# Kernel optimization log

Hardware: AMD Instinct MI355X
Metric: run time of the kernel (lower is better)

The kernel has to match this reference:

```python
import jax, jax.numpy as jnp
import numpy as np

NODE_DIM = 256
HIDDEN = 64
NUM_REL = 10
N_NODES = 100000
N_EDGES = 1600000


def _linear_params(key, fan_in, fan_out):
    kw, kb = jax.random.split(key)
    bound = 1.0 / np.sqrt(fan_in)
    W = jax.random.uniform(kw, (fan_in, fan_out), minval=-bound, maxval=bound, dtype=jnp.float32)
    b = jax.random.uniform(kb, (fan_out,), minval=-bound, maxval=bound, dtype=jnp.float32)
    return W, b


def setup_inputs() -> dict:
    key = jax.random.key(0)
    ks = jax.random.split(key, 6)
    x = jax.random.normal(ks[0], (N_NODES, NODE_DIM), dtype=jnp.float32)
    edge_index = jax.random.randint(ks[1], (2, N_EDGES), 0, N_NODES, dtype=jnp.int32)
    W1, b1 = _linear_params(ks[2], NODE_DIM, HIDDEN)   # node_encoder layer 1
    W2, b2 = _linear_params(ks[3], HIDDEN, HIDDEN)     # node_encoder layer 2
    W3, b3 = _linear_params(ks[4], 2 * HIDDEN, HIDDEN) # relation_mlp layer 1
    W4, b4 = _linear_params(ks[5], HIDDEN, NUM_REL)    # relation_mlp layer 2
    return {"x": x, "edge_index": edge_index,
            "W1": W1, "b1": b1, "W2": W2, "b2": b2,
            "W3": W3, "b3": b3, "W4": W4, "b4": b4}


def reference(x, edge_index, W1, b1, W2, b2, W3, b3, W4, b4):
    # node encoder: Linear -> ReLU -> Linear, [N, node_dim] -> [N, H]
    h = jax.nn.relu(x @ W1 + b1) @ W2 + b2
    row, col = edge_index[0], edge_index[1]
    # gather + concat: [E, 2H]
    edge_features = jnp.concatenate([h[row], h[col]], axis=-1)
    # relation MLP: [E, 2H] -> [E, num_relations]
    relation_logits = jax.nn.relu(edge_features @ W3 + b3) @ W4 + b4
    relation_probs = jax.nn.softmax(relation_logits, axis=-1)
    edge_type = jnp.argmax(relation_logits, axis=-1)
    return edge_type, relation_probs
```

## Files before the change

### kernel.cpp

```cpp
#include <hip/hip_runtime.h>

#define NODE_DIM 256
#define HIDDEN 64
#define NUM_REL 10

#define FMA4(A, S, W) do { \
    (A).x = fmaf((S), (W).x, (A).x); \
    (A).y = fmaf((S), (W).y, (A).y); \
    (A).z = fmaf((S), (W).z, (A).z); \
    (A).w = fmaf((S), (W).w, (A).w); } while (0)

#define ELEM(V, I) ((I) == 0 ? (V).x : (I) == 1 ? (V).y : (I) == 2 ? (V).z : (V).w)

__global__ __launch_bounds__(256) void node_kernel(
    const float* __restrict__ x,
    const float* __restrict__ W1, const float* __restrict__ b1,
    const float* __restrict__ W2, const float* __restrict__ b2,
    const float* __restrict__ W3,
    float* __restrict__ Hout, float* __restrict__ Aout, int N)
{
    int n = blockIdx.x * 256 + threadIdx.x;
    if (n >= N) return;

    float h1[64];
    #pragma unroll
    for (int j = 0; j < 64; ++j) h1[j] = 0.0f;

    const float4* xr = (const float4*)(x + (size_t)n * NODE_DIM);
    #pragma unroll 1
    for (int k4 = 0; k4 < NODE_DIM / 4; ++k4) {
        float4 xv = xr[k4];
        const float* w = W1 + (size_t)k4 * 4 * 64;
        #pragma unroll
        for (int j = 0; j < 64; ++j) h1[j] = fmaf(xv.x, w[j], h1[j]);
        #pragma unroll
        for (int j = 0; j < 64; ++j) h1[j] = fmaf(xv.y, w[64 + j], h1[j]);
        #pragma unroll
        for (int j = 0; j < 64; ++j) h1[j] = fmaf(xv.z, w[128 + j], h1[j]);
        #pragma unroll
        for (int j = 0; j < 64; ++j) h1[j] = fmaf(xv.w, w[192 + j], h1[j]);
    }
    #pragma unroll
    for (int j = 0; j < 64; ++j) h1[j] = fmaxf(h1[j] + b1[j], 0.0f);

    float h[64];
    #pragma unroll
    for (int c = 0; c < 4; ++c) {
        float acc[16];
        #pragma unroll
        for (int j = 0; j < 16; ++j) acc[j] = 0.0f;
        #pragma unroll
        for (int k = 0; k < 64; ++k) {
            const float* w = W2 + (size_t)k * 64 + c * 16;
            #pragma unroll
            for (int j = 0; j < 16; ++j) acc[j] = fmaf(h1[k], w[j], acc[j]);
        }
        #pragma unroll
        for (int j = 0; j < 16; ++j) h[c * 16 + j] = acc[j] + b2[c * 16 + j];
    }

    float4* hr = (float4*)(Hout + (size_t)n * 64);
    #pragma unroll
    for (int j4 = 0; j4 < 16; ++j4) {
        float4 v;
        v.x = h[4 * j4]; v.y = h[4 * j4 + 1];
        v.z = h[4 * j4 + 2]; v.w = h[4 * j4 + 3];
        hr[j4] = v;
    }

    float4* ar = (float4*)(Aout + (size_t)n * 64);
    #pragma unroll
    for (int c = 0; c < 4; ++c) {
        float acc[16];
        #pragma unroll
        for (int j = 0; j < 16; ++j) acc[j] = 0.0f;
        #pragma unroll
        for (int k = 0; k < 64; ++k) {
            const float* w = W3 + (size_t)k * 64 + c * 16;
            #pragma unroll
            for (int j = 0; j < 16; ++j) acc[j] = fmaf(h[k], w[j], acc[j]);
        }
        #pragma unroll
        for (int j4 = 0; j4 < 4; ++j4) {
            float4 v;
            v.x = acc[4 * j4]; v.y = acc[4 * j4 + 1];
            v.z = acc[4 * j4 + 2]; v.w = acc[4 * j4 + 3];
            ar[c * 4 + j4] = v;
        }
    }
}

__global__ __launch_bounds__(256, 4) void edge_kernel(
    const int* __restrict__ ei,
    const float* __restrict__ H, const float* __restrict__ A,
    const float* __restrict__ W3, const float* __restrict__ b3,
    const float* __restrict__ W4, const float* __restrict__ b4,
    float* __restrict__ out_type, float* __restrict__ out_probs, int E)
{
    __shared__ float4 HcS[256 * 8];

    const int tid = threadIdx.x;
    const int e = blockIdx.x * 256 + tid;
    const bool valid = (e < E);
    const int sw = tid & 7;
    float4* myscr = &HcS[tid * 8];

    const int c = valid ? ei[E + e] : 0;
    const int r = valid ? ei[e] : 0;
    const float4* src = (const float4*)(H + (size_t)c * 64);
    const float4* Ar  = (const float4*)(A + (size_t)r * 64);

    #pragma unroll
    for (int q = 0; q < 8; ++q) myscr[q ^ sw] = src[q];

    float4 acc[16];
    #pragma unroll
    for (int j = 0; j < 16; ++j) acc[j] = Ar[j];

    const float* W3b = W3 + 64 * 64;

    #pragma unroll 1
    for (int k4 = 0; k4 < 8; ++k4) {
        const float4 hv = myscr[k4 ^ sw];
        #pragma unroll
        for (int i = 0; i < 4; ++i) {
            const float s = ELEM(hv, i);
            const float* w = W3b + (size_t)(k4 * 4 + i) * 64;
            #pragma unroll
            for (int j = 0; j < 16; ++j) {
                float4 wv = *(const float4*)(w + 4 * j);
                FMA4(acc[j], s, wv);
            }
        }
    }

    #pragma unroll
    for (int q = 0; q < 8; ++q) myscr[q ^ sw] = src[8 + q];

    #pragma unroll 1
    for (int k4 = 8; k4 < 16; ++k4) {
        const float4 hv = myscr[(k4 - 8) ^ sw];
        #pragma unroll
        for (int i = 0; i < 4; ++i) {
            const float s = ELEM(hv, i);
            const float* w = W3b + (size_t)(k4 * 4 + i) * 64;
            #pragma unroll
            for (int j = 0; j < 16; ++j) {
                float4 wv = *(const float4*)(w + 4 * j);
                FMA4(acc[j], s, wv);
            }
        }
    }

    #pragma unroll
    for (int j = 0; j < 16; ++j) {
        float4 bv = *(const float4*)(b3 + 4 * j);
        acc[j].x = fmaxf(acc[j].x + bv.x, 0.f);
        acc[j].y = fmaxf(acc[j].y + bv.y, 0.f);
        acc[j].z = fmaxf(acc[j].z + bv.z, 0.f);
        acc[j].w = fmaxf(acc[j].w + bv.w, 0.f);
    }

    float lg[NUM_REL];
    #pragma unroll
    for (int j = 0; j < NUM_REL; ++j) lg[j] = 0.0f;
    #pragma unroll
    for (int jq = 0; jq < 16; ++jq) {
        #pragma unroll
        for (int i = 0; i < 4; ++i) {
            const float s = ELEM(acc[jq], i);
            const float* w = W4 + (size_t)(jq * 4 + i) * NUM_REL;
            #pragma unroll
            for (int j = 0; j < NUM_REL; ++j) lg[j] = fmaf(s, w[j], lg[j]);
        }
    }

    if (!valid) return;

    #pragma unroll
    for (int j = 0; j < NUM_REL; ++j) lg[j] += b4[j];

    int best = 0;
    float bm = lg[0];
    #pragma unroll
    for (int j = 1; j < NUM_REL; ++j)
        if (lg[j] > bm) { bm = lg[j]; best = j; }

    float p[NUM_REL];
    float sum = 0.0f;
    #pragma unroll
    for (int j = 0; j < NUM_REL; ++j) {
        p[j] = expf(lg[j] - bm);
        sum += p[j];
    }
    float inv = 1.0f / sum;

    out_type[e] = (float)best;
    float* op = out_probs + (size_t)e * NUM_REL;
    #pragma unroll
    for (int j = 0; j < NUM_REL; ++j) op[j] = p[j] * inv;
}

extern "C" void kernel_launch(void* const* d_in, const int* in_sizes, int n_in,
                              void* d_out, int out_size, void* d_ws, size_t ws_size,
                              hipStream_t stream)
{
    const float* x  = (const float*)d_in[0];
    const int*   ei = (const int*)d_in[1];
    const float* W1 = (const float*)d_in[2];
    const float* b1 = (const float*)d_in[3];
    const float* W2 = (const float*)d_in[4];
    const float* b2 = (const float*)d_in[5];
    const float* W3 = (const float*)d_in[6];
    const float* b3 = (const float*)d_in[7];
    const float* W4 = (const float*)d_in[8];
    const float* b4 = (const float*)d_in[9];

    int N = in_sizes[0] / NODE_DIM;
    int E = in_sizes[1] / 2;

    float* H = (float*)d_ws;
    float* A = H + (size_t)N * 64;

    int nb = (N + 255) / 256;
    int eb = (E + 255) / 256;

    float* out_type  = (float*)d_out;
    float* out_probs = (float*)d_out + E;

    hipLaunchKernelGGL(node_kernel, dim3(nb), dim3(256), 0, stream,
                       x, W1, b1, W2, b2, W3, H, A, N);
    hipLaunchKernelGGL(edge_kernel, dim3(eb), dim3(256), 0, stream,
                       ei, H, A, W3, b3, W4, b4, out_type, out_probs, E);
}
```

Measured before the change: 323.8 us.

## Split node-encoder outputs across four waves per node tile using shared memory

```diff
diff --git a/kernel.cpp b/kernel.cpp
--- a/kernel.cpp
+++ b/kernel.cpp
@@ -12,81 +12,96 @@
 
 #define ELEM(V, I) ((I) == 0 ? (V).x : (I) == 1 ? (V).y : (I) == 2 ? (V).z : (V).w)
 
-__global__ __launch_bounds__(256) void node_kernel(
+__global__ __launch_bounds__(256, 4) void node_kernel(
     const float* __restrict__ x,
     const float* __restrict__ W1, const float* __restrict__ b1,
     const float* __restrict__ W2, const float* __restrict__ b2,
     const float* __restrict__ W3,
     float* __restrict__ Hout, float* __restrict__ Aout, int N)
 {
-    int n = blockIdx.x * 256 + threadIdx.x;
-    if (n >= N) return;
-
-    float h1[64];
-    #pragma unroll
-    for (int j = 0; j < 64; ++j) h1[j] = 0.0f;
-
-    const float4* xr = (const float4*)(x + (size_t)n * NODE_DIM);
+    __shared__ float h1s[64][65];
+    __shared__ float hs[64][65];
+
+    const int tid  = threadIdx.x;
+    const int wv   = tid >> 6;
+    const int lane = tid & 63;
+    const int jb   = wv * 16;
+    const int n    = blockIdx.x * 64 + lane;
+    const bool valid = (n < N);
+    const int nc   = valid ? n : (N - 1);
+
+    float4 a0 = make_float4(0.f, 0.f, 0.f, 0.f);
+    float4 a1 = a0, a2 = a0, a3 = a0;
+
+    const float4* xr = (const float4*)(x + (size_t)nc * NODE_DIM);
     #pragma unroll 1
     for (int k4 = 0; k4 < NODE_DIM / 4; ++k4) {
         float4 xv = xr[k4];
-        const float* w = W1 + (size_t)k4 * 4 * 64;
-        #pragma unroll
-        for (int j = 0; j < 64; ++j) h1[j] = fmaf(xv.x, w[j], h1[j]);
-        #pragma unroll
-        for (int j = 0; j < 64; ++j) h1[j] = fmaf(xv.y, w[64 + j], h1[j]);
-        #pragma unroll
-        for (int j = 0; j < 64; ++j) h1[j] = fmaf(xv.z, w[128 + j], h1[j]);
-        #pragma unroll
-        for (int j = 0; j < 64; ++j) h1[j] = fmaf(xv.w, w[192 + j], h1[j]);
-    }
-    #pragma unroll
-    for (int j = 0; j < 64; ++j) h1[j] = fmaxf(h1[j] + b1[j], 0.0f);
-
-    float h[64];
-    #pragma unroll
-    for (int c = 0; c < 4; ++c) {
-        float acc[16];
-        #pragma unroll
-        for (int j = 0; j < 16; ++j) acc[j] = 0.0f;
-        #pragma unroll
-        for (int k = 0; k < 64; ++k) {
-            const float* w = W2 + (size_t)k * 64 + c * 16;
-            #pragma unroll
-            for (int j = 0; j < 16; ++j) acc[j] = fmaf(h1[k], w[j], acc[j]);
-        }
-        #pragma unroll
-        for (int j = 0; j < 16; ++j) h[c * 16 + j] = acc[j] + b2[c * 16 + j];
-    }
-
-    float4* hr = (float4*)(Hout + (size_t)n * 64);
-    #pragma unroll
-    for (int j4 = 0; j4 < 16; ++j4) {
-        float4 v;
-        v.x = h[4 * j4]; v.y = h[4 * j4 + 1];
-        v.z = h[4 * j4 + 2]; v.w = h[4 * j4 + 3];
-        hr[j4] = v;
-    }
-
-    float4* ar = (float4*)(Aout + (size_t)n * 64);
-    #pragma unroll
-    for (int c = 0; c < 4; ++c) {
-        float acc[16];
-        #pragma unroll
-        for (int j = 0; j < 16; ++j) acc[j] = 0.0f;
-        #pragma unroll
-        for (int k = 0; k < 64; ++k) {
-            const float* w = W3 + (size_t)k * 64 + c * 16;
-            #pragma unroll
-            for (int j = 0; j < 16; ++j) acc[j] = fmaf(h[k], w[j], acc[j]);
-        }
-        #pragma unroll
-        for (int j4 = 0; j4 < 4; ++j4) {
-            float4 v;
-            v.x = acc[4 * j4]; v.y = acc[4 * j4 + 1];
-            v.z = acc[4 * j4 + 2]; v.w = acc[4 * j4 + 3];
-            ar[c * 4 + j4] = v;
-        }
+        #pragma unroll
+        for (int i = 0; i < 4; ++i) {
+            float s = ELEM(xv, i);
+            const float4* w = (const float4*)(W1 + (size_t)(k4 * 4 + i) * 64 + jb);
+            float4 w0 = w[0], w1 = w[1], w2 = w[2], w3 = w[3];
+            FMA4(a0, s, w0); FMA4(a1, s, w1);
+            FMA4(a2, s, w2); FMA4(a3, s, w3);
+        }
+    }
+    {
+        const float4* bv = (const float4*)(b1 + jb);
+        float4 b0 = bv[0], b1v = bv[1], b2v = bv[2], b3v = bv[3];
+        float* d = &h1s[lane][jb];
+        d[0]  = fmaxf(a0.x + b0.x, 0.f);  d[1]  = fmaxf(a0.y + b0.y, 0.f);
+        d[2]  = fmaxf(a0.z + b0.z, 0.f);  d[3]  = fmaxf(a0.w + b0.w, 0.f);
+        d[4]  = fmaxf(a1.x + b1v.x, 0.f); d[5]  = fmaxf(a1.y + b1v.y, 0.f);
+        d[6]  = fmaxf(a1.z + b1v.z, 0.f); d[7]  = fmaxf(a1.w + b1v.w, 0.f);
+        d[8]  = fmaxf(a2.x + b2v.x, 0.f); d[9]  = fmaxf(a2.y + b2v.y, 0.f);
+        d[10] = fmaxf(a2.z + b2v.z, 0.f); d[11] = fmaxf(a2.w + b2v.w, 0.f);
+        d[12] = fmaxf(a3.x + b3v.x, 0.f); d[13] = fmaxf(a3.y + b3v.y, 0.f);
+        d[14] = fmaxf(a3.z + b3v.z, 0.f); d[15] = fmaxf(a3.w + b3v.w, 0.f);
+    }
+    __syncthreads();
+
+    a0 = make_float4(0.f, 0.f, 0.f, 0.f); a1 = a0; a2 = a0; a3 = a0;
+    #pragma unroll 1
+    for (int k = 0; k < 64; ++k) {
+        float s = h1s[lane][k];
+        const float4* w = (const float4*)(W2 + (size_t)k * 64 + jb);
+        float4 w0 = w[0], w1 = w[1], w2 = w[2], w3 = w[3];
+        FMA4(a0, s, w0); FMA4(a1, s, w1);
+        FMA4(a2, s, w2); FMA4(a3, s, w3);
+    }
+    {
+        const float4* bv = (const float4*)(b2 + jb);
+        float4 b0 = bv[0], b1v = bv[1], b2v = bv[2], b3v = bv[3];
+        float4 r0, r1, r2, r3;
+        r0.x = a0.x + b0.x;  r0.y = a0.y + b0.y;  r0.z = a0.z + b0.z;  r0.w = a0.w + b0.w;
+        r1.x = a1.x + b1v.x; r1.y = a1.y + b1v.y; r1.z = a1.z + b1v.z; r1.w = a1.w + b1v.w;
+        r2.x = a2.x + b2v.x; r2.y = a2.y + b2v.y; r2.z = a2.z + b2v.z; r2.w = a2.w + b2v.w;
+        r3.x = a3.x + b3v.x; r3.y = a3.y + b3v.y; r3.z = a3.z + b3v.z; r3.w = a3.w + b3v.w;
+        float* d = &hs[lane][jb];
+        d[0]  = r0.x; d[1]  = r0.y; d[2]  = r0.z; d[3]  = r0.w;
+        d[4]  = r1.x; d[5]  = r1.y; d[6]  = r1.z; d[7]  = r1.w;
+        d[8]  = r2.x; d[9]  = r2.y; d[10] = r2.z; d[11] = r2.w;
+        d[12] = r3.x; d[13] = r3.y; d[14] = r3.z; d[15] = r3.w;
+        if (valid) {
+            float4* g = (float4*)(Hout + (size_t)n * 64 + jb);
+            g[0] = r0; g[1] = r1; g[2] = r2; g[3] = r3;
+        }
+    }
+    __syncthreads();
+
+    a0 = make_float4(0.f, 0.f, 0.f, 0.f); a1 = a0; a2 = a0; a3 = a0;
+    #pragma unroll 1
+    for (int k = 0; k < 64; ++k) {
+        float s = hs[lane][k];
+        const float4* w = (const float4*)(W3 + (size_t)k * 64 + jb);
+        float4 w0 = w[0], w1 = w[1], w2 = w[2], w3 = w[3];
+        FMA4(a0, s, w0); FMA4(a1, s, w1);
+        FMA4(a2, s, w2); FMA4(a3, s, w3);
+    }
+    if (valid) {
+        float4* g = (float4*)(Aout + (size_t)n * 64 + jb);
+        g[0] = a0; g[1] = a1; g[2] = a2; g[3] = a3;
     }
 }
 
@@ -222,7 +237,7 @@
     float* H = (float*)d_ws;
     float* A = H + (size_t)N * 64;
 
-    int nb = (N + 255) / 256;
+    int nb = (N + 63) / 64;
     int eb = (E + 255) / 256;
 
     float* out_type  = (float*)d_out;
```

Measured after the change: 535.7 us. +65.5%, slower.

## Split fused node MLP into three column-sliced GEMM launches

Applied to the files above, without the earlier changes.

```diff
diff --git a/kernel.cpp b/kernel.cpp
--- a/kernel.cpp
+++ b/kernel.cpp
@@ -12,82 +12,54 @@
 
 #define ELEM(V, I) ((I) == 0 ? (V).x : (I) == 1 ? (V).y : (I) == 2 ? (V).z : (V).w)
 
-__global__ __launch_bounds__(256) void node_kernel(
-    const float* __restrict__ x,
-    const float* __restrict__ W1, const float* __restrict__ b1,
-    const float* __restrict__ W2, const float* __restrict__ b2,
-    const float* __restrict__ W3,
-    float* __restrict__ Hout, float* __restrict__ Aout, int N)
+__global__ __launch_bounds__(256) void gemm_slice(
+    const float* __restrict__ in, int K,
+    const float* __restrict__ W, const float* __restrict__ bias,
+    int relu, float* __restrict__ out, int N)
 {
-    int n = blockIdx.x * 256 + threadIdx.x;
+    const int n  = blockIdx.x * 256 + threadIdx.x;
+    const int jb = blockIdx.y * 16;
     if (n >= N) return;
 
-    float h1[64];
-    #pragma unroll
-    for (int j = 0; j < 64; ++j) h1[j] = 0.0f;
-
-    const float4* xr = (const float4*)(x + (size_t)n * NODE_DIM);
+    float4 a0 = make_float4(0.f, 0.f, 0.f, 0.f);
+    float4 a1 = a0, a2 = a0, a3 = a0;
+
+    const float4* inr = (const float4*)(in + (size_t)n * K);
+    const int K4 = K >> 2;
     #pragma unroll 1
-    for (int k4 = 0; k4 < NODE_DIM / 4; ++k4) {
-        float4 xv = xr[k4];
-        const float* w = W1 + (size_t)k4 * 4 * 64;
-        #pragma unroll
-        for (int j = 0; j < 64; ++j) h1[j] = fmaf(xv.x, w[j], h1[j]);
-        #pragma unroll
-        for (int j = 0; j < 64; ++j) h1[j] = fmaf(xv.y, w[64 + j], h1[j]);
-        #pragma unroll
-        for (int j = 0; j < 64; ++j) h1[j] = fmaf(xv.z, w[128 + j], h1[j]);
-        #pragma unroll
-        for (int j = 0; j < 64; ++j) h1[j] = fmaf(xv.w, w[192 + j], h1[j]);
-    }
-    #pragma unroll
-    for (int j = 0; j < 64; ++j) h1[j] = fmaxf(h1[j] + b1[j], 0.0f);
-
-    float h[64];
-    #pragma unroll
-    for (int c = 0; c < 4; ++c) {
-        float acc[16];
-        #pragma unroll
-        for (int j = 0; j < 16; ++j) acc[j] = 0.0f;
-        #pragma unroll
-        for (int k = 0; k < 64; ++k) {
-            const float* w = W2 + (size_t)k * 64 + c * 16;
-            #pragma unroll
-            for (int j = 0; j < 16; ++j) acc[j] = fmaf(h1[k], w[j], acc[j]);
-        }
-        #pragma unroll
-        for (int j = 0; j < 16; ++j) h[c * 16 + j] = acc[j] + b2[c * 16 + j];
-    }
-
-    float4* hr = (float4*)(Hout + (size_t)n * 64);
-    #pragma unroll
-    for (int j4 = 0; j4 < 16; ++j4) {
-        float4 v;
-        v.x = h[4 * j4]; v.y = h[4 * j4 + 1];
-        v.z = h[4 * j4 + 2]; v.w = h[4 * j4 + 3];
-        hr[j4] = v;
-    }
-
-    float4* ar = (float4*)(Aout + (size_t)n * 64);
-    #pragma unroll
-    for (int c = 0; c < 4; ++c) {
-        float acc[16];
-        #pragma unroll
-        for (int j = 0; j < 16; ++j) acc[j] = 0.0f;
-        #pragma unroll
-        for (int k = 0; k < 64; ++k) {
-            const float* w = W3 + (size_t)k * 64 + c * 16;
-            #pragma unroll
-            for (int j = 0; j < 16; ++j) acc[j] = fmaf(h[k], w[j], acc[j]);
-        }
-        #pragma unroll
-        for (int j4 = 0; j4 < 4; ++j4) {
-            float4 v;
-            v.x = acc[4 * j4]; v.y = acc[4 * j4 + 1];
-            v.z = acc[4 * j4 + 2]; v.w = acc[4 * j4 + 3];
-            ar[c * 4 + j4] = v;
-        }
-    }
+    for (int k4 = 0; k4 < K4; ++k4) {
+        float4 xv = inr[k4];
+        #pragma unroll
+        for (int i = 0; i < 4; ++i) {
+            const float s = ELEM(xv, i);
+            const float4* w = (const float4*)(W + (size_t)(k4 * 4 + i) * 64 + jb);
+            float4 w0 = w[0], w1 = w[1], w2 = w[2], w3 = w[3];
+            FMA4(a0, s, w0); FMA4(a1, s, w1);
+            FMA4(a2, s, w2); FMA4(a3, s, w3);
+        }
+    }
+
+    if (bias) {
+        const float4* bv = (const float4*)(bias + jb);
+        float4 b0 = bv[0], b1v = bv[1], b2v = bv[2], b3v = bv[3];
+        a0.x += b0.x;  a0.y += b0.y;  a0.z += b0.z;  a0.w += b0.w;
+        a1.x += b1v.x; a1.y += b1v.y; a1.z += b1v.z; a1.w += b1v.w;
+        a2.x += b2v.x; a2.y += b2v.y; a2.z += b2v.z; a2.w += b2v.w;
+        a3.x += b3v.x; a3.y += b3v.y; a3.z += b3v.z; a3.w += b3v.w;
+    }
+    if (relu) {
+        a0.x = fmaxf(a0.x, 0.f); a0.y = fmaxf(a0.y, 0.f);
+        a0.z = fmaxf(a0.z, 0.f); a0.w = fmaxf(a0.w, 0.f);
+        a1.x = fmaxf(a1.x, 0.f); a1.y = fmaxf(a1.y, 0.f);
+        a1.z = fmaxf(a1.z, 0.f); a1.w = fmaxf(a1.w, 0.f);
+        a2.x = fmaxf(a2.x, 0.f); a2.y = fmaxf(a2.y, 0.f);
+        a2.z = fmaxf(a2.z, 0.f); a2.w = fmaxf(a2.w, 0.f);
+        a3.x = fmaxf(a3.x, 0.f); a3.y = fmaxf(a3.y, 0.f);
+        a3.z = fmaxf(a3.z, 0.f); a3.w = fmaxf(a3.w, 0.f);
+    }
+
+    float4* g = (float4*)(out + (size_t)n * 64 + jb);
+    g[0] = a0; g[1] = a1; g[2] = a2; g[3] = a3;
 }
 
 __global__ __launch_bounds__(256, 4) void edge_kernel(
@@ -219,17 +191,23 @@
     int N = in_sizes[0] / NODE_DIM;
     int E = in_sizes[1] / 2;
 
-    float* H = (float*)d_ws;
-    float* A = H + (size_t)N * 64;
+    float* H  = (float*)d_ws;
+    float* A  = H + (size_t)N * 64;
+    float* H1 = H + 2 * (size_t)N * 64;
 
     int nb = (N + 255) / 256;
     int eb = (E + 255) / 256;
+    dim3 ngrid(nb, 4);
 
     float* out_type  = (float*)d_out;
     float* out_probs = (float*)d_out + E;
 
-    hipLaunchKernelGGL(node_kernel, dim3(nb), dim3(256), 0, stream,
-                       x, W1, b1, W2, b2, W3, H, A, N);
+    hipLaunchKernelGGL(gemm_slice, ngrid, dim3(256), 0, stream,
+                       x, NODE_DIM, W1, b1, 1, H1, N);
+    hipLaunchKernelGGL(gemm_slice, ngrid, dim3(256), 0, stream,
+                       H1, HIDDEN, W2, b2, 0, H, N);
+    hipLaunchKernelGGL(gemm_slice, ngrid, dim3(256), 0, stream,
+                       H, HIDDEN, W3, (const float*)nullptr, 0, A, N);
     hipLaunchKernelGGL(edge_kernel, dim3(eb), dim3(256), 0, stream,
                        ei, H, A, W3, b3, W4, b4, out_type, out_probs, E);
 }
```

New measurement: 842.6 us. 2.6x slower.
